# Optimization experiments

Measured on AMD Instinct MI355X. Metric: run time of the kernel, lower is better.

The kernel has to match this reference:

```python
import jax, jax.numpy as jnp
import numpy as np

N, F, T, H = 1024, 22, 1000, 64
EPS = 1e-5


def setup_inputs() -> dict:
    key = jax.random.key(0)
    ks = iter(jax.random.split(key, 64))
    def rn(shape, s=0.1):
        return jax.random.normal(next(ks), shape, jnp.float32) * s
    inp = {"x": rn((N, F, T), 1.0)}
    in_dims = [F, H, H]
    for l in range(3):
        inp[f"Wih{l}"] = rn((4 * H, in_dims[l]))
        inp[f"Whh{l}"] = rn((4 * H, H))
        inp[f"bih{l}"] = rn((4 * H,))
        inp[f"bhh{l}"] = rn((4 * H,))
    fc = [(64, 54), (54, 44), (44, 24), (24, 4)]
    for i, (di, do) in enumerate(fc):
        inp[f"w{i}"] = rn((do, di))
        inp[f"b{i}"] = rn((do,))
    for i, d in enumerate([54, 44, 24]):
        inp[f"g{i}"] = jnp.ones((d,), jnp.float32)
        inp[f"be{i}"] = jnp.zeros((d,), jnp.float32)
        inp[f"m{i}"] = rn((d,))
        inp[f"v{i}"] = jax.random.uniform(next(ks), (d,), jnp.float32) + 0.5
    return inp


def _lstm_layer(xs, Wih, Whh, b):
    # xs: (T, N, in) -> hs: (T, N, H)
    n = xs.shape[1]
    h0 = jnp.zeros((n, Whh.shape[1]), xs.dtype)
    def step(carry, xt):
        h, c = carry
        z = xt @ Wih.T + h @ Whh.T + b  # (N, 4H)
        i, f, g, o = jnp.split(z, 4, axis=-1)  # PyTorch gate order i,f,g,o
        c = jax.nn.sigmoid(f) * c + jax.nn.sigmoid(i) * jnp.tanh(g)
        h = jax.nn.sigmoid(o) * jnp.tanh(c)
        return (h, c), h
    (_, _), hs = jax.lax.scan(step, (h0, h0), xs)
    return hs


def _bn(x, g, be, m, v):
    return (x - m) * jax.lax.rsqrt(v + EPS) * g + be


def reference(x, Wih0, Whh0, bih0, bhh0, Wih1, Whh1, bih1, bhh1,
              Wih2, Whh2, bih2, bhh2,
              w0, b0, g0, be0, m0, v0,
              w1, b1, g1, be1, m1, v1,
              w2, b2, g2, be2, m2, v2,
              w3, b3):
    # (N, F, T) -> permute(0,2,1) -> (N, T, F); scan over time-major (T, N, F)
    xs = jnp.transpose(x, (2, 0, 1))
    xs = _lstm_layer(xs, Wih0, Whh0, bih0 + bhh0)
    xs = _lstm_layer(xs, Wih1, Whh1, bih1 + bhh1)
    xs = _lstm_layer(xs, Wih2, Whh2, bih2 + bhh2)
    h = xs[-1]  # last timestep, (N, H)
    h = jax.nn.relu(_bn(h @ w0.T + b0, g0, be0, m0, v0))
    h = jax.nn.relu(_bn(h @ w1.T + b1, g1, be1, m1, v1))
    h = jax.nn.relu(_bn(h @ w2.T + b2, g2, be2, m2, v2))
    return h @ w3.T + b3
```

## Files before the change

### kernel.cpp

```cpp
#include <hip/hip_runtime.h>
#include <hip/hip_fp16.h>

#define TT 1000
#define FF 22
#define HH 64
#define BB 4
#define NBLK 256
#define S0 112
#define S1 144
#define SL0 (4 * S0)
#define SL1 (4 * S1)

typedef _Float16 half8 __attribute__((ext_vector_type(8)));
typedef float float4v __attribute__((ext_vector_type(4)));

__device__ __forceinline__ float sel4(const float4v a, int q) {
    float lo = (q & 2) ? a[2] : a[0];
    float hi = (q & 2) ? a[3] : a[1];
    return (q & 1) ? hi : lo;
}

__device__ __forceinline__ float gate_fused(const float z[4], float& c) {
    float e0 = __expf(-z[0]);
    float e1 = __expf(-z[1]);
    float e2 = __expf(2.0f * z[2]);
    float d1 = 1.0f + e1;
    float d2 = (1.0f + e0) * (1.0f + e2);
    float r  = __builtin_amdgcn_rcpf(d1 * d2);
    float f  = d2 * r;
    float ig = (e2 - 1.0f) * (d1 * r);
    float cc = __builtin_fmaf(f, c, ig);
    c = cc;
    float e3 = __expf(-z[3]);
    float e4 = __expf(2.0f * cc);
    float r2 = __builtin_amdgcn_rcpf((1.0f + e3) * (1.0f + e4));
    return (e4 - 1.0f) * r2;
}

#define SYNC() do { asm volatile("s_waitcnt lgkmcnt(0)" ::: "memory"); \
                    __builtin_amdgcn_s_barrier(); \
                    asm volatile("" ::: "memory"); } while (0)
#define SB()   __builtin_amdgcn_sched_barrier(0)

extern "C" __global__ void __launch_bounds__(896, 1)
lstm_fused(const float* __restrict__ x,
           const float* __restrict__ Wih0, const float* __restrict__ Whh0,
           const float* __restrict__ bih0, const float* __restrict__ bhh0,
           const float* __restrict__ Wih1, const float* __restrict__ Whh1,
           const float* __restrict__ bih1, const float* __restrict__ bhh1,
           const float* __restrict__ Wih2, const float* __restrict__ Whh2,
           const float* __restrict__ bih2, const float* __restrict__ bhh2,
           const float* __restrict__ w0, const float* __restrict__ b0,
           const float* __restrict__ w1, const float* __restrict__ b1,
           const float* __restrict__ w2, const float* __restrict__ b2,
           const float* __restrict__ w3, const float* __restrict__ b3,
           const float* __restrict__ g0, const float* __restrict__ be0,
           const float* __restrict__ m0, const float* __restrict__ v0,
           const float* __restrict__ g1, const float* __restrict__ be1,
           const float* __restrict__ m1, const float* __restrict__ v1,
           const float* __restrict__ g2, const float* __restrict__ be2,
           const float* __restrict__ m2, const float* __restrict__ v2,
           float* __restrict__ out)
{
    __shared__ __align__(16) _Float16 in0[8 * SL0];
    __shared__ __align__(16) _Float16 in1[8 * SL1];
    __shared__ __align__(16) _Float16 in2[8 * SL1];
    __shared__ float fcA[BB * 64];
    __shared__ float fcB[BB * 64];
    __shared__ float fcW[54 * 65];
    __shared__ float fcP[5 * 64];

    const int tid  = threadIdx.x;
    const int wv   = tid >> 6;
    const int role = wv >> 2;
    const int w4   = wv & 3;
    const int l    = tid & 63;
    const int q    = l >> 4;
    const int l15  = l & 15;
    const int u    = 16 * w4 + l15;
    const int b    = q;
    const int n0   = blockIdx.x * BB;

    for (int i = tid; i < 8 * SL0; i += 896) in0[i] = (_Float16)0.0f;
    for (int i = tid; i < 8 * SL1; i += 896) in1[i] = (_Float16)0.0f;
    for (int i = tid; i < 8 * SL1; i += 896) in2[i] = (_Float16)0.0f;

    half8 wf[4][4];
    float bv[4];
    if (role == 2) {
#pragma unroll
        for (int g = 0; g < 4; ++g) {
            const int row = 64 * g + u;
#pragma unroll
            for (int kt = 0; kt < 3; ++kt) {
                half8 h{};
#pragma unroll
                for (int j = 0; j < 8; ++j) {
                    const int k = 32 * kt + 8 * q + j;
                    float val = 0.0f;
                    if (k < 32) { if (k < FF) val = Wih0[row * FF + k]; }
                    else        { val = Whh0[row * HH + (k - 32)]; }
                    h[j] = (_Float16)val;
                }
                wf[g][kt] = h;
            }
            wf[g][3] = half8{};
            bv[g] = bih0[row] + bhh0[row];
        }
    } else if (role < 2) {
        const float* Wih = role ? Wih1 : Wih2;
        const float* Whh = role ? Whh1 : Whh2;
        const float* bih = role ? bih1 : bih2;
        const float* bhh = role ? bhh1 : bhh2;
#pragma unroll
        for (int g = 0; g < 4; ++g) {
            const int row = 64 * g + u;
#pragma unroll
            for (int kt = 0; kt < 4; ++kt) {
                half8 h{};
#pragma unroll
                for (int j = 0; j < 8; ++j) {
                    const int k = 32 * kt + 8 * q + j;
                    h[j] = (_Float16)((k < 64) ? Wih[row * HH + k] : Whh[row * HH + (k - 64)]);
                }
                wf[g][kt] = h;
            }
            bv[g] = bih[row] + bhh[row];
        }
    }

    const int  st  = tid - 768;
    const bool xok = (role == 3) && (st >= 0) && (st < BB * FF);
    const int  xb  = xok ? (st / FF) : 0;
    const int  xf  = xok ? (st - xb * FF) : 0;
    const float* xp = x + ((size_t)(n0 + xb) * FF + xf) * TT;

    __syncthreads();

    if (xok) {
        in0[0 * SL0 + xb * S0 + xf] = (_Float16)xp[0];
        in0[1 * SL0 + xb * S0 + xf] = (_Float16)xp[1];
    }
    float xA = xok ? xp[2] : 0.f;
    float xB = xok ? xp[3] : 0.f;

    __syncthreads();

    const int arow = (role == 2) ? ((l15 & 3) * S0 + q * 8) : ((l15 & 3) * S1 + q * 8);
    float c = 0.f;
    const float4v zz = {0.f, 0.f, 0.f, 0.f};
    float4v acc[4] = {zz, zz, zz, zz};

    if (role == 2) {
        half8 f0 = *(const half8*)(in0 + 0 * SL0 + arow);
#pragma unroll
        for (int g = 0; g < 4; ++g)
            acc[g] = __builtin_amdgcn_mfma_f32_16x16x32_f16(f0, wf[g][0], zz, 0, 0, 0);
    }

    for (int k = 0; k < 126; ++k) {
#pragma unroll
        for (int s = 0; s < 8; ++s) {
            const int tau = 8 * k + s;
            SYNC();

            if (role == 3) {
                if (tau <= TT - 3) {
                    if (xok) in0[((s + 2) & 7) * SL0 + xb * S0 + xf] = (_Float16)xA;
                    xA = xB;
                    if (xok) {
                        int tn = tau + 4; if (tn > TT - 1) tn = TT - 1;
                        xB = xp[tn];
                    }
                }
            } else if (role == 2) {
                const bool act  = (tau <= TT - 1);
                const bool actn = (tau <= TT - 2);
                half8 f0{};
                if (act) {
                    const _Float16* rd = in0 + s * SL0;
                    half8 r1 = *(const half8*)(rd + arow + 32);
                    half8 r2 = *(const half8*)(rd + arow + 64);
#pragma unroll
                    for (int g = 0; g < 4; ++g)
                        acc[g] = __builtin_amdgcn_mfma_f32_16x16x32_f16(r1, wf[g][1], acc[g], 0, 0, 0);
#pragma unroll
                    for (int g = 0; g < 4; ++g)
                        acc[g] = __builtin_amdgcn_mfma_f32_16x16x32_f16(r2, wf[g][2], acc[g], 0, 0, 0);
                }
                if (actn)
                    f0 = *(const half8*)(in0 + ((s + 1) & 7) * SL0 + arow);
                if (act) {
                    float z[4];
#pragma unroll
                    for (int g = 0; g < 4; ++g) z[g] = sel4(acc[g], q) + bv[g];
                    float h = gate_fused(z, c);
                    _Float16 hf = (_Float16)h;
                    in0[((s + 1) & 7) * SL0 + b * S0 + 32 + u] = hf;
                    in1[s * SL1 + b * S1 + u]                  = hf;
                }
                if (actn) {
#pragma unroll
                    for (int g = 0; g < 4; ++g)
                        acc[g] = __builtin_amdgcn_mfma_f32_16x16x32_f16(f0, wf[g][0], zz, 0, 0, 0);
                }
            } else if (role == 1) {
                const bool act  = (tau >= 2) && (tau <= TT + 1);
                const bool actn = (tau >= 1) && (tau <= TT);
                half8 f0{}, f1{};
                if (act) {
                    const _Float16* rr = in1 + ((s + 6) & 7) * SL1;
                    half8 r2 = *(const half8*)(rr + arow + 64);
                    half8 r3 = *(const half8*)(rr + arow + 96);
#pragma unroll
                    for (int g = 0; g < 4; ++g)
                        acc[g] = __builtin_amdgcn_mfma_f32_16x16x32_f16(r2, wf[g][2], acc[g], 0, 0, 0);
#pragma unroll
                    for (int g = 0; g < 4; ++g)
                        acc[g] = __builtin_amdgcn_mfma_f32_16x16x32_f16(r3, wf[g][3], acc[g], 0, 0, 0);
                }
                if (actn) {
                    const _Float16* rn = in1 + ((s + 7) & 7) * SL1;
                    f0 = *(const half8*)(rn + arow);
                    f1 = *(const half8*)(rn + arow + 32);
                }
                if (act) {
                    float z[4];
#pragma unroll
                    for (int g = 0; g < 4; ++g) z[g] = sel4(acc[g], q) + bv[g];
                    float h = gate_fused(z, c);
                    _Float16 hf = (_Float16)h;
                    in1[((s + 7) & 7) * SL1 + b * S1 + 64 + u] = hf;
                    in2[((s + 6) & 7) * SL1 + b * S1 + u]      = hf;
                }
                if (actn) {
#pragma unroll
                    for (int g = 0; g < 4; ++g)
                        acc[g] = __builtin_amdgcn_mfma_f32_16x16x32_f16(f0, wf[g][0], zz, 0, 0, 0);
#pragma unroll
                    for (int g = 0; g < 4; ++g)
                        acc[g] = __builtin_amdgcn_mfma_f32_16x16x32_f16(f1, wf[g][1], acc[g], 0, 0, 0);
                }
            } else {
                const bool act  = (tau >= 4) && (tau <= TT + 3);
                const bool actn = (tau >= 3) && (tau <= TT + 2);
                half8 f0{}, f1{};
                if (act) {
                    const _Float16* rr = in2 + ((s + 4) & 7) * SL1;
                    half8 r2 = *(const half8*)(rr + arow + 64);
                    half8 r3 = *(const half8*)(rr + arow + 96);
#pragma unroll
                    for (int g = 0; g < 4; ++g)
                        acc[g] = __builtin_amdgcn_mfma_f32_16x16x32_f16(r2, wf[g][2], acc[g], 0, 0, 0);
#pragma unroll
                    for (int g = 0; g < 4; ++g)
                        acc[g] = __builtin_amdgcn_mfma_f32_16x16x32_f16(r3, wf[g][3], acc[g], 0, 0, 0);
                }
                if (actn) {
                    const _Float16* rn = in2 + ((s + 5) & 7) * SL1;
                    f0 = *(const half8*)(rn + arow);
                    f1 = *(const half8*)(rn + arow + 32);
                }
                if (act) {
                    float z[4];
#pragma unroll
                    for (int g = 0; g < 4; ++g) z[g] = sel4(acc[g], q) + bv[g];
                    float h = gate_fused(z, c);
                    if (tau != TT + 3) {
                        in2[((s + 5) & 7) * SL1 + b * S1 + 64 + u] = (_Float16)h;
                    } else {
                        fcA[b * 64 + u] = h;
                    }
                }
                if (actn) {
#pragma unroll
                    for (int g = 0; g < 4; ++g)
                        acc[g] = __builtin_amdgcn_mfma_f32_16x16x32_f16(f0, wf[g][0], zz, 0, 0, 0);
#pragma unroll
                    for (int g = 0; g < 4; ++g)
                        acc[g] = __builtin_amdgcn_mfma_f32_16x16x32_f16(f1, wf[g][1], acc[g], 0, 0, 0);
                }
            }
            SB();
        }
    }

    __syncthreads();

    for (int i = tid; i < 54 * 64; i += 896) fcW[(i >> 6) * 65 + (i & 63)] = w0[i];
    for (int i = tid; i < 54; i += 896) {
        fcP[i] = b0[i]; fcP[64 + i] = g0[i]; fcP[128 + i] = be0[i];
        fcP[192 + i] = m0[i]; fcP[256 + i] = v0[i];
    }
    __syncthreads();
    for (int idx = tid; idx < BB * 54; idx += 896) {
        const int bb = idx / 54, j = idx - bb * 54;
        float s = fcP[j];
        for (int k = 0; k < 64; ++k) s += fcW[j * 65 + k] * fcA[bb * 64 + k];
        s = (s - fcP[192 + j]) * rsqrtf(fcP[256 + j] + 1e-5f) * fcP[64 + j] + fcP[128 + j];
        fcB[bb * 64 + j] = fmaxf(s, 0.0f);
    }
    __syncthreads();

    for (int i = tid; i < 44 * 54; i += 896) fcW[(i / 54) * 55 + (i % 54)] = w1[i];
    for (int i = tid; i < 44; i += 896) {
        fcP[i] = b1[i]; fcP[64 + i] = g1[i]; fcP[128 + i] = be1[i];
        fcP[192 + i] = m1[i]; fcP[256 + i] = v1[i];
    }
    __syncthreads();
    for (int idx = tid; idx < BB * 44; idx += 896) {
        const int bb = idx / 44, j = idx - bb * 44;
        float s = fcP[j];
        for (int k = 0; k < 54; ++k) s += fcW[j * 55 + k] * fcB[bb * 64 + k];
        s = (s - fcP[192 + j]) * rsqrtf(fcP[256 + j] + 1e-5f) * fcP[64 + j] + fcP[128 + j];
        fcA[bb * 64 + j] = fmaxf(s, 0.0f);
    }
    __syncthreads();

    for (int i = tid; i < 24 * 44; i += 896) fcW[(i / 44) * 45 + (i % 44)] = w2[i];
    for (int i = tid; i < 24; i += 896) {
        fcP[i] = b2[i]; fcP[64 + i] = g2[i]; fcP[128 + i] = be2[i];
        fcP[192 + i] = m2[i]; fcP[256 + i] = v2[i];
    }
    __syncthreads();
    for (int idx = tid; idx < BB * 24; idx += 896) {
        const int bb = idx / 24, j = idx - bb * 24;
        float s = fcP[j];
        for (int k = 0; k < 44; ++k) s += fcW[j * 45 + k] * fcA[bb * 64 + k];
        s = (s - fcP[192 + j]) * rsqrtf(fcP[256 + j] + 1e-5f) * fcP[64 + j] + fcP[128 + j];
        fcB[bb * 64 + j] = fmaxf(s, 0.0f);
    }
    __syncthreads();

    for (int i = tid; i < 4 * 24; i += 896) fcW[(i / 24) * 25 + (i % 24)] = w3[i];
    for (int i = tid; i < 4; i += 896) fcP[i] = b3[i];
    __syncthreads();
    for (int idx = tid; idx < BB * 4; idx += 896) {
        const int bb = idx / 4, j = idx - bb * 4;
        float s = fcP[j];
        for (int k = 0; k < 24; ++k) s += fcW[j * 25 + k] * fcB[bb * 64 + k];
        out[(size_t)(n0 + bb) * 4 + j] = s;
    }
}

extern "C" void kernel_launch(void* const* d_in, const int* in_sizes, int n_in,
                              void* d_out, int out_size, void* d_ws, size_t ws_size,
                              hipStream_t stream) {
    const float* p[33];
    for (int i = 0; i < 33; ++i) p[i] = (const float*)d_in[i];
    lstm_fused<<<NBLK, 896, 0, stream>>>(
        p[0],
        p[1], p[2], p[3], p[4],
        p[5], p[6], p[7], p[8],
        p[9], p[10], p[11], p[12],
        p[13], p[14], p[15], p[16], p[17], p[18], p[19], p[20],
        p[21], p[22], p[23], p[24],
        p[25], p[26], p[27], p[28],
        p[29], p[30], p[31], p[32],
        (float*)d_out);
}
```

Measured before the change: 780.9 us.

## Batch layer 1/2 input projections over four timesteps and shuffle results via bpermute

Layers 1 and 2 previously computed their input-to-hidden projection for one timestep per step. They now compute it once every four steps, with each MFMA row-group covering a different timestep. The results are redistributed across lanes with ds_bpermute transposes into register buffers, so the per-step critical path only runs the recurrent MFMAs. This deepens the pipeline skew between layers (more steps, larger lag) and drops the sched_barrier. In exchange it adds cross-lane permutes, extra registers and a longer prologue and epilogue.

```diff
diff --git a/kernel.cpp b/kernel.cpp
--- a/kernel.cpp
+++ b/kernel.cpp
@@ -37,10 +37,33 @@
     return (e4 - 1.0f) * r2;
 }
 
+__device__ __forceinline__ float bperm(int idx4, float v) {
+    return __int_as_float(__builtin_amdgcn_ds_bpermute(idx4, __float_as_int(v)));
+}
+
+__device__ __forceinline__ void transp4(float4v& w, float4v f, bool qo, bool qh,
+                                        int i16, int i32) {
+    float s10 = bperm(i16, f[1]);
+    float s11 = bperm(i16, f[0]);
+    float s12 = bperm(i16, f[3]);
+    float s13 = bperm(i16, f[2]);
+    float b0 = qo ? s10 : f[0];
+    float b1 = qo ? f[1] : s11;
+    float b2 = qo ? s12 : f[2];
+    float b3 = qo ? f[3] : s13;
+    float s20 = bperm(i32, b2);
+    float s21 = bperm(i32, b3);
+    float s22 = bperm(i32, b0);
+    float s23 = bperm(i32, b1);
+    w[0] = qh ? s20 : b0;
+    w[1] = qh ? s21 : b1;
+    w[2] = qh ? b2 : s22;
+    w[3] = qh ? b3 : s23;
+}
+
 #define SYNC() do { asm volatile("s_waitcnt lgkmcnt(0)" ::: "memory"); \
                     __builtin_amdgcn_s_barrier(); \
                     asm volatile("" ::: "memory"); } while (0)
-#define SB()   __builtin_amdgcn_sched_barrier(0)
 
 extern "C" __global__ void __launch_bounds__(896, 1)
 lstm_fused(const float* __restrict__ x,
@@ -146,19 +169,21 @@
 
     __syncthreads();
 
-    const int arow = (role == 2) ? ((l15 & 3) * S0 + q * 8) : ((l15 & 3) * S1 + q * 8);
+    const int fb    = (l15 & 3) * ((role == 2) ? S0 : S1) + q * 8;
+    const int soff  = l15 >> 2;
+    const int i16   = ((l ^ 16) << 2);
+    const int i32   = ((l ^ 32) << 2);
+    const bool qo   = (q & 1) != 0;
+    const bool qh   = (q & 2) != 0;
     float c = 0.f;
     const float4v zz = {0.f, 0.f, 0.f, 0.f};
-    float4v acc[4] = {zz, zz, zz, zz};
-
-    if (role == 2) {
-        half8 f0 = *(const half8*)(in0 + 0 * SL0 + arow);
-#pragma unroll
-        for (int g = 0; g < 4; ++g)
-            acc[g] = __builtin_amdgcn_mfma_f32_16x16x32_f16(f0, wf[g][0], zz, 0, 0, 0);
-    }
-
-    for (int k = 0; k < 126; ++k) {
+    float4v W0[4] = {zz, zz, zz, zz};
+    float4v W1[4] = {zz, zz, zz, zz};
+    float4v biasC[4];
+#pragma unroll
+    for (int g = 0; g < 4; ++g) biasC[g] = float4v{bv[g], bv[g], bv[g], bv[g]};
+
+    for (int k = 0; k < 127; ++k) {
 #pragma unroll
         for (int s = 0; s < 8; ++s) {
             const int tau = 8 * k + s;
@@ -174,114 +199,120 @@
                     }
                 }
             } else if (role == 2) {
-                const bool act  = (tau <= TT - 1);
-                const bool actn = (tau <= TT - 2);
-                half8 f0{};
-                if (act) {
+                if (tau <= TT - 1) {
                     const _Float16* rd = in0 + s * SL0;
-                    half8 r1 = *(const half8*)(rd + arow + 32);
-                    half8 r2 = *(const half8*)(rd + arow + 64);
-#pragma unroll
-                    for (int g = 0; g < 4; ++g)
-                        acc[g] = __builtin_amdgcn_mfma_f32_16x16x32_f16(r1, wf[g][1], acc[g], 0, 0, 0);
-#pragma unroll
-                    for (int g = 0; g < 4; ++g)
-                        acc[g] = __builtin_amdgcn_mfma_f32_16x16x32_f16(r2, wf[g][2], acc[g], 0, 0, 0);
-                }
-                if (actn)
-                    f0 = *(const half8*)(in0 + ((s + 1) & 7) * SL0 + arow);
-                if (act) {
+                    half8 a0 = *(const half8*)(rd + fb);
+                    half8 a1 = *(const half8*)(rd + fb + 32);
+                    half8 a2 = *(const half8*)(rd + fb + 64);
+                    float4v A[4];
+#pragma unroll
+                    for (int g = 0; g < 4; ++g)
+                        A[g] = __builtin_amdgcn_mfma_f32_16x16x32_f16(a0, wf[g][0], biasC[g], 0, 0, 0);
+#pragma unroll
+                    for (int g = 0; g < 4; ++g)
+                        A[g] = __builtin_amdgcn_mfma_f32_16x16x32_f16(a1, wf[g][1], A[g], 0, 0, 0);
+#pragma unroll
+                    for (int g = 0; g < 4; ++g)
+                        A[g] = __builtin_amdgcn_mfma_f32_16x16x32_f16(a2, wf[g][2], A[g], 0, 0, 0);
                     float z[4];
 #pragma unroll
-                    for (int g = 0; g < 4; ++g) z[g] = sel4(acc[g], q) + bv[g];
+                    for (int g = 0; g < 4; ++g) z[g] = sel4(A[g], q);
                     float h = gate_fused(z, c);
                     _Float16 hf = (_Float16)h;
                     in0[((s + 1) & 7) * SL0 + b * S0 + 32 + u] = hf;
                     in1[s * SL1 + b * S1 + u]                  = hf;
                 }
-                if (actn) {
-#pragma unroll
-                    for (int g = 0; g < 4; ++g)
-                        acc[g] = __builtin_amdgcn_mfma_f32_16x16x32_f16(f0, wf[g][0], zz, 0, 0, 0);
-                }
             } else if (role == 1) {
-                const bool act  = (tau >= 2) && (tau <= TT + 1);
-                const bool actn = (tau >= 1) && (tau <= TT);
-                half8 f0{}, f1{};
-                if (act) {
-                    const _Float16* rr = in1 + ((s + 6) & 7) * SL1;
-                    half8 r2 = *(const half8*)(rr + arow + 64);
-                    half8 r3 = *(const half8*)(rr + arow + 96);
-#pragma unroll
-                    for (int g = 0; g < 4; ++g)
-                        acc[g] = __builtin_amdgcn_mfma_f32_16x16x32_f16(r2, wf[g][2], acc[g], 0, 0, 0);
-#pragma unroll
-                    for (int g = 0; g < 4; ++g)
-                        acc[g] = __builtin_amdgcn_mfma_f32_16x16x32_f16(r3, wf[g][3], acc[g], 0, 0, 0);
-                }
-                if (actn) {
-                    const _Float16* rn = in1 + ((s + 7) & 7) * SL1;
-                    f0 = *(const half8*)(rn + arow);
-                    f1 = *(const half8*)(rn + arow + 32);
-                }
-                if (act) {
+                if (s == 0 || s == 4) {
+                    if (tau >= 4 && tau <= TT) {
+                        const int sl = (s + 4 + soff) & 7;
+                        const _Float16* fp = in1 + sl * SL1 + fb;
+                        half8 fa0 = *(const half8*)(fp);
+                        half8 fa1 = *(const half8*)(fp + 32);
+                        float4v F[4];
+#pragma unroll
+                        for (int g = 0; g < 4; ++g)
+                            F[g] = __builtin_amdgcn_mfma_f32_16x16x32_f16(fa0, wf[g][0], biasC[g], 0, 0, 0);
+#pragma unroll
+                        for (int g = 0; g < 4; ++g)
+                            F[g] = __builtin_amdgcn_mfma_f32_16x16x32_f16(fa1, wf[g][1], F[g], 0, 0, 0);
+#pragma unroll
+                        for (int g = 0; g < 4; ++g) {
+                            if (s == 0) transp4(W0[g], F[g], qo, qh, i16, i32);
+                            else        transp4(W1[g], F[g], qo, qh, i16, i32);
+                        }
+                    }
+                }
+                if (tau >= 6 && tau <= TT + 5) {
+                    const _Float16* rr = in1 + ((s + 2) & 7) * SL1;
+                    half8 r2 = *(const half8*)(rr + fb + 64);
+                    half8 r3 = *(const half8*)(rr + fb + 96);
+                    float4v A[4];
+#pragma unroll
+                    for (int g = 0; g < 4; ++g)
+                        A[g] = __builtin_amdgcn_mfma_f32_16x16x32_f16(r2, wf[g][2], zz, 0, 0, 0);
+#pragma unroll
+                    for (int g = 0; g < 4; ++g)
+                        A[g] = __builtin_amdgcn_mfma_f32_16x16x32_f16(r3, wf[g][3], A[g], 0, 0, 0);
                     float z[4];
-#pragma unroll
-                    for (int g = 0; g < 4; ++g) z[g] = sel4(acc[g], q) + bv[g];
+                    const int ri = (s + 2) & 3;
+#pragma unroll
+                    for (int g = 0; g < 4; ++g) {
+                        const float fw = (s >= 2 && s <= 5) ? W0[g][ri] : W1[g][ri];
+                        z[g] = sel4(A[g], q) + fw;
+                    }
                     float h = gate_fused(z, c);
                     _Float16 hf = (_Float16)h;
-                    in1[((s + 7) & 7) * SL1 + b * S1 + 64 + u] = hf;
-                    in2[((s + 6) & 7) * SL1 + b * S1 + u]      = hf;
-                }
-                if (actn) {
-#pragma unroll
-                    for (int g = 0; g < 4; ++g)
-                        acc[g] = __builtin_amdgcn_mfma_f32_16x16x32_f16(f0, wf[g][0], zz, 0, 0, 0);
-#pragma unroll
-                    for (int g = 0; g < 4; ++g)
-                        acc[g] = __builtin_amdgcn_mfma_f32_16x16x32_f16(f1, wf[g][1], acc[g], 0, 0, 0);
+                    in1[((s + 3) & 7) * SL1 + b * S1 + 64 + u] = hf;
+                    in2[((s + 2) & 7) * SL1 + b * S1 + u]      = hf;
                 }
             } else {
-                const bool act  = (tau >= 4) && (tau <= TT + 3);
-                const bool actn = (tau >= 3) && (tau <= TT + 2);
-                half8 f0{}, f1{};
-                if (act) {
+                if (s == 2 || s == 6) {
+                    if (tau >= 10 && tau <= TT + 6) {
+                        const int sl = (s + 6 + soff) & 7;
+                        const _Float16* fp = in2 + sl * SL1 + fb;
+                        half8 fa0 = *(const half8*)(fp);
+                        half8 fa1 = *(const half8*)(fp + 32);
+                        float4v F[4];
+#pragma unroll
+                        for (int g = 0; g < 4; ++g)
+                            F[g] = __builtin_amdgcn_mfma_f32_16x16x32_f16(fa0, wf[g][0], biasC[g], 0, 0, 0);
+#pragma unroll
+                        for (int g = 0; g < 4; ++g)
+                            F[g] = __builtin_amdgcn_mfma_f32_16x16x32_f16(fa1, wf[g][1], F[g], 0, 0, 0);
+#pragma unroll
+                        for (int g = 0; g < 4; ++g) {
+                            if (s == 2) transp4(W0[g], F[g], qo, qh, i16, i32);
+                            else        transp4(W1[g], F[g], qo, qh, i16, i32);
+                        }
+                    }
+                }
+                if (tau >= 12 && tau <= TT + 11) {
                     const _Float16* rr = in2 + ((s + 4) & 7) * SL1;
-                    half8 r2 = *(const half8*)(rr + arow + 64);
-                    half8 r3 = *(const half8*)(rr + arow + 96);
-#pragma unroll
-                    for (int g = 0; g < 4; ++g)
-                        acc[g] = __builtin_amdgcn_mfma_f32_16x16x32_f16(r2, wf[g][2], acc[g], 0, 0, 0);
-#pragma unroll
-                    for (int g = 0; g < 4; ++g)
-                        acc[g] = __builtin_amdgcn_mfma_f32_16x16x32_f16(r3, wf[g][3], acc[g], 0, 0, 0);
-                }
-                if (actn) {
-                    const _Float16* rn = in2 + ((s + 5) & 7) * SL1;
-                    f0 = *(const half8*)(rn + arow);
-                    f1 = *(const half8*)(rn + arow + 32);
-                }
-                if (act) {
+                    half8 r2 = *(const half8*)(rr + fb + 64);
+                    half8 r3 = *(const half8*)(rr + fb + 96);
+                    float4v A[4];
+#pragma unroll
+                    for (int g = 0; g < 4; ++g)
+                        A[g] = __builtin_amdgcn_mfma_f32_16x16x32_f16(r2, wf[g][2], zz, 0, 0, 0);
+#pragma unroll
+                    for (int g = 0; g < 4; ++g)
+                        A[g] = __builtin_amdgcn_mfma_f32_16x16x32_f16(r3, wf[g][3], A[g], 0, 0, 0);
                     float z[4];
-#pragma unroll
-                    for (int g = 0; g < 4; ++g) z[g] = sel4(acc[g], q) + bv[g];
+                    const int ri = s & 3;
+#pragma unroll
+                    for (int g = 0; g < 4; ++g) {
+                        const float fw = (s >= 4) ? W0[g][ri] : W1[g][ri];
+                        z[g] = sel4(A[g], q) + fw;
+                    }
                     float h = gate_fused(z, c);
-                    if (tau != TT + 3) {
+                    if (tau != TT + 11) {
                         in2[((s + 5) & 7) * SL1 + b * S1 + 64 + u] = (_Float16)h;
                     } else {
                         fcA[b * 64 + u] = h;
                     }
                 }
-                if (actn) {
-#pragma unroll
-                    for (int g = 0; g < 4; ++g)
-                        acc[g] = __builtin_amdgcn_mfma_f32_16x16x32_f16(f0, wf[g][0], zz, 0, 0, 0);
-#pragma unroll
-                    for (int g = 0; g < 4; ++g)
-                        acc[g] = __builtin_amdgcn_mfma_f32_16x16x32_f16(f1, wf[g][1], acc[g], 0, 0, 0);
-                }
             }
-            SB();
         }
     }
 
```

Result: slower. 2.038 ms (+160.9%).
